# Kernel optimization log

Measured on AMD Instinct MI355X. Metric: run time of the kernel, lower is better.

The kernel has to match this reference:

```python
import jax, jax.numpy as jnp
import numpy as np

K = 7
PAD = 3
SIZE = K * K
MAX_STEP = 2
IMG_SIZE = 384
EPS = 1e-5


def _unfold(x, k, pad):
    # x: (n, c, h, w) -> (n, c, k*k, h*w), same layout as F.unfold with stride 1
    n, c, h, w = x.shape
    xp = jnp.pad(x, ((0, 0), (0, 0), (pad, pad), (pad, pad)))
    patches = jnp.stack(
        [xp[:, :, i:i + h, j:j + w] for i in range(k) for j in range(k)], axis=2
    )  # (n, c, k*k, h, w)
    return patches.reshape(n, c, k * k, h * w)


def setup_inputs() -> dict:
    key = jax.random.key(0)
    k1, k2, k3, k4 = jax.random.split(key, 4)
    n, c, h, w = 1, 256, 96, 96
    inputs = {
        "input": jax.random.normal(k1, (n, c, h, w), dtype=jnp.float32),
        "weight": jax.random.uniform(k2, (n, SIZE, h * w), dtype=jnp.float32),
        "conv_w": jax.random.normal(k3, (3, c), dtype=jnp.float32) * 0.05,
        "conv_b": jax.random.normal(k4, (3,), dtype=jnp.float32) * 0.05,
    }
    return inputs


def reference(input, weight, conv_w, conv_b):
    n, c, h, w = input.shape
    wc = weight.shape[1] // SIZE  # 1 -> broadcasts over channels
    wgt = weight.reshape(n, wc, SIZE, h * w)
    # row-normalize per-pixel window weights (sym_norm=False branch)
    norm_weight = wgt / (jnp.sum(wgt, axis=2, keepdims=True) + EPS)
    x = input
    for _ in range(MAX_STEP):
        p = _unfold(x, K, PAD)                  # (n, c, k*k, h*w)
        x = (p * norm_weight).sum(axis=2).reshape(n, c, h, w)
    # 1x1 conv latent_dim -> 3
    x = jnp.einsum("nchw,oc->nohw", x, conv_w) + conv_b[None, :, None, None]
    # bilinear upsample, half-pixel centers (== torch align_corners=False)
    x = jax.image.resize(x, (n, 3, IMG_SIZE, IMG_SIZE), method="bilinear")
    return x
```

## Files before the change

kernel.cpp:

```cpp
#include <hip/hip_runtime.h>

#define HW 9216
#define W 96
#define H 96
#define NC 256
#define NT 49
#define EPSV 1e-5f

#define TS 16
#define HSZ 22
#define CC 8
#define NZ (NC / CC)

typedef _Float16 half8 __attribute__((ext_vector_type(8)));

template <int FUSE_CONV>
__global__ __launch_bounds__(256) void step_kernel(const float* __restrict__ x,
                                                   const float* __restrict__ w,
                                                   const float* __restrict__ cw,
                                                   float* __restrict__ y) {
    __shared__ half8 xs[HSZ][HSZ];
    const int tx = threadIdx.x & 15;
    const int ty = threadIdx.x >> 4;
    const int bx = blockIdx.x * TS;
    const int by = blockIdx.y * TS;
    const int px = bx + tx;
    const int py = by + ty;
    const int p = py * W + px;

    float wreg[NT];
    float s = 0.f;
#pragma unroll
    for (int t = 0; t < NT; ++t) { wreg[t] = w[t * HW + p]; s += wreg[t]; }
    const float inv = 1.f / (s + EPSV);
#pragma unroll
    for (int t = 0; t < NT; ++t) wreg[t] *= inv;

    const int cbase = blockIdx.z * CC;
    const float* __restrict__ xb = x + cbase * HW;
    for (int i = threadIdx.x; i < HSZ * HSZ; i += 256) {
        int hy = i / HSZ;
        int hx = i - hy * HSZ;
        int gy = by - 3 + hy;
        int gx = bx - 3 + hx;
        half8 h;
#pragma unroll
        for (int c = 0; c < 8; ++c) h[c] = (_Float16)0.f;
        if ((unsigned)gy < (unsigned)H && (unsigned)gx < (unsigned)W) {
            const float* sp = xb + gy * W + gx;
#pragma unroll
            for (int c = 0; c < 8; ++c) h[c] = (_Float16)sp[c * HW];
        }
        xs[hy][hx] = h;
    }
    __syncthreads();

    float acc[8];
#pragma unroll
    for (int k = 0; k < 8; ++k) acc[k] = 0.f;

#pragma unroll
    for (int i = 0; i < 7; ++i) {
#pragma unroll
        for (int j = 0; j < 7; ++j) {
            const float wv = wreg[i * 7 + j];
            const half8 v = xs[ty + i][tx + j];
#pragma unroll
            for (int k = 0; k < 8; ++k)
                acc[k] = fmaf((float)v[k], wv, acc[k]);
        }
    }

    if (FUSE_CONV) {
        float o0 = 0.f, o1 = 0.f, o2 = 0.f;
#pragma unroll
        for (int k = 0; k < 8; ++k) {
            const int c = cbase + k;
            o0 = fmaf(acc[k], cw[c], o0);
            o1 = fmaf(acc[k], cw[NC + c], o1);
            o2 = fmaf(acc[k], cw[2 * NC + c], o2);
        }
        const int z = blockIdx.z;
        y[(z * 3 + 0) * HW + p] = o0;
        y[(z * 3 + 1) * HW + p] = o1;
        y[(z * 3 + 2) * HW + p] = o2;
    } else {
#pragma unroll
        for (int k = 0; k < 8; ++k)
            y[(cbase + k) * HW + p] = acc[k];
    }
}

#define OUTS 384
#define SRCP 10
__global__ __launch_bounds__(256) void upsample_kernel(const float* __restrict__ partial,
                                                       const float* __restrict__ cb,
                                                       float* __restrict__ dst) {
    __shared__ float cvs[3][SRCP][SRCP];
    const int X = blockIdx.x * 32;
    const int Y = blockIdx.y * 32;
    const int x0s = X >> 2;
    const int y0s = Y >> 2;

    for (int e = threadIdx.x; e < 3 * SRCP * SRCP; e += 256) {
        int ch = e / (SRCP * SRCP);
        int r = e - ch * (SRCP * SRCP);
        int sy = r / SRCP;
        int sx = r - sy * SRCP;
        int gy = min(max(y0s - 1 + sy, 0), H - 1);
        int gx = min(max(x0s - 1 + sx, 0), W - 1);
        const int p = gy * W + gx;
        float sum = cb[ch];
#pragma unroll
        for (int z = 0; z < NZ; ++z) sum += partial[(z * 3 + ch) * HW + p];
        cvs[ch][sy][sx] = sum;
    }
    __syncthreads();

    const int xl = threadIdx.x & 31;
    const int yl0 = threadIdx.x >> 5;
    const int xo = X + xl;
    const float sxf = xo * 0.25f - 0.375f;
    const float fxf = floorf(sxf);
    const int jx = (int)fxf - (x0s - 1);
    const float fx = sxf - fxf;

#pragma unroll
    for (int k = 0; k < 4; ++k) {
        const int yo = Y + yl0 + 8 * k;
        const float syf = yo * 0.25f - 0.375f;
        const float fyf = floorf(syf);
        const int jy = (int)fyf - (y0s - 1);
        const float fy = syf - fyf;
#pragma unroll
        for (int ch = 0; ch < 3; ++ch) {
            const float v00 = cvs[ch][jy][jx], v01 = cvs[ch][jy][jx + 1];
            const float v10 = cvs[ch][jy + 1][jx], v11 = cvs[ch][jy + 1][jx + 1];
            const float v0 = v00 + (v01 - v00) * fx;
            const float v1 = v10 + (v11 - v10) * fx;
            dst[ch * OUTS * OUTS + yo * OUTS + xo] = v0 + (v1 - v0) * fy;
        }
    }
}

extern "C" void kernel_launch(void* const* d_in, const int* in_sizes, int n_in,
                              void* d_out, int out_size, void* d_ws, size_t ws_size,
                              hipStream_t stream) {
    const float* input  = (const float*)d_in[0];
    const float* weight = (const float*)d_in[1];
    const float* conv_w = (const float*)d_in[2];
    const float* conv_b = (const float*)d_in[3];
    float* out = (float*)d_out;

    float* ws = (float*)d_ws;
    float* x1      = ws;
    float* partial = x1 + NC * HW;

    dim3 g(W / TS, H / TS, NZ);
    step_kernel<0><<<g, 256, 0, stream>>>(input, weight, nullptr, x1);
    step_kernel<1><<<g, 256, 0, stream>>>(x1, weight, conv_w, partial);

    dim3 gu(OUTS / 32, OUTS / 32);
    upsample_kernel<<<gu, 256, 0, stream>>>(partial, conv_b, out);
}
```

Measured before the change: 35.59 us.

## Prepack inputs and normalized weights to fp16 in a separate pre-pass kernel

Adds a pack kernel that converts the input to a channel-interleaved fp16 layout (8 channels per pixel) and precomputes the normalized window weights once as fp16 pairs. The step kernels then load halo tiles with one 16-byte vector load per pixel instead of eight strided fp32 loads, and they no longer recompute weight normalization in each of the 64 blocks per pixel. The intermediate after the first step is stored in fp16. The cost is an extra kernel launch and pass over the input, plus reduced weight precision from fp16 rounding.

```diff
diff --git a/kernel.cpp b/kernel.cpp
--- a/kernel.cpp
+++ b/kernel.cpp
@@ -5,20 +5,52 @@
 #define H 96
 #define NC 256
 #define NT 49
+#define NPAIR 25
 #define EPSV 1e-5f
 
 #define TS 16
 #define HSZ 22
 #define CC 8
-#define NZ (NC / CC)
+#define NZ 32
 
 typedef _Float16 half8 __attribute__((ext_vector_type(8)));
+typedef _Float16 half2v __attribute__((ext_vector_type(2)));
+
+__global__ __launch_bounds__(256) void pack_kernel(const float* __restrict__ x,
+                                                   const float* __restrict__ w,
+                                                   _Float16* __restrict__ xpack,
+                                                   half2v* __restrict__ nwh) {
+    if (blockIdx.y < 8) {
+        const int g = blockIdx.y * 4 + (threadIdx.x >> 6);
+        const int px = blockIdx.x * 64 + (threadIdx.x & 63);
+        const float* __restrict__ sp = x + (size_t)(g * 8) * HW + px;
+        half8 h;
+#pragma unroll
+        for (int c = 0; c < 8; ++c) h[c] = (_Float16)sp[c * HW];
+        *(half8*)(xpack + ((size_t)g * HW + px) * 8) = h;
+    } else {
+        if (blockIdx.x >= 36) return;
+        const int p = blockIdx.x * 256 + threadIdx.x;
+        float wv[NT];
+        float s = 0.f;
+#pragma unroll
+        for (int t = 0; t < NT; ++t) { wv[t] = w[t * HW + p]; s += wv[t]; }
+        const float inv = 1.f / (s + EPSV);
+#pragma unroll
+        for (int i = 0; i < NPAIR; ++i) {
+            half2v h;
+            h[0] = (_Float16)(wv[2 * i] * inv);
+            h[1] = (2 * i + 1 < NT) ? (_Float16)(wv[2 * i + 1] * inv) : (_Float16)0.f;
+            nwh[i * HW + p] = h;
+        }
+    }
+}
 
 template <int FUSE_CONV>
-__global__ __launch_bounds__(256) void step_kernel(const float* __restrict__ x,
-                                                   const float* __restrict__ w,
+__global__ __launch_bounds__(256) void step_kernel(const _Float16* __restrict__ xin,
+                                                   const half2v* __restrict__ nwh,
                                                    const float* __restrict__ cw,
-                                                   float* __restrict__ y) {
+                                                   void* __restrict__ yout) {
     __shared__ half8 xs[HSZ][HSZ];
     const int tx = threadIdx.x & 15;
     const int ty = threadIdx.x >> 4;
@@ -27,31 +59,28 @@
     const int px = bx + tx;
     const int py = by + ty;
     const int p = py * W + px;
-
-    float wreg[NT];
-    float s = 0.f;
-#pragma unroll
-    for (int t = 0; t < NT; ++t) { wreg[t] = w[t * HW + p]; s += wreg[t]; }
-    const float inv = 1.f / (s + EPSV);
-#pragma unroll
-    for (int t = 0; t < NT; ++t) wreg[t] *= inv;
-
-    const int cbase = blockIdx.z * CC;
-    const float* __restrict__ xb = x + cbase * HW;
-    for (int i = threadIdx.x; i < HSZ * HSZ; i += 256) {
-        int hy = i / HSZ;
-        int hx = i - hy * HSZ;
-        int gy = by - 3 + hy;
-        int gx = bx - 3 + hx;
-        half8 h;
-#pragma unroll
-        for (int c = 0; c < 8; ++c) h[c] = (_Float16)0.f;
-        if ((unsigned)gy < (unsigned)H && (unsigned)gx < (unsigned)W) {
-            const float* sp = xb + gy * W + gx;
-#pragma unroll
-            for (int c = 0; c < 8; ++c) h[c] = (_Float16)sp[c * HW];
-        }
-        xs[hy][hx] = h;
+    const int z = blockIdx.z;
+
+    half2v wu[NPAIR];
+#pragma unroll
+    for (int i = 0; i < NPAIR; ++i) wu[i] = nwh[i * HW + p];
+
+    const _Float16* __restrict__ xz = xin + (size_t)z * HW * 8;
+#pragma unroll
+    for (int it = 0; it < 2; ++it) {
+        const int i = threadIdx.x + it * 256;
+        if (i < HSZ * HSZ) {
+            const int hy = i / HSZ;
+            const int hx = i - hy * HSZ;
+            const int gy = by - 3 + hy;
+            const int gx = bx - 3 + hx;
+            half8 v;
+#pragma unroll
+            for (int c = 0; c < 8; ++c) v[c] = (_Float16)0.f;
+            if ((unsigned)gy < (unsigned)H && (unsigned)gx < (unsigned)W)
+                v = *(const half8*)(xz + (size_t)(gy * W + gx) * 8);
+            xs[hy][hx] = v;
+        }
     }
     __syncthreads();
 
@@ -63,16 +92,18 @@
     for (int i = 0; i < 7; ++i) {
 #pragma unroll
         for (int j = 0; j < 7; ++j) {
-            const float wv = wreg[i * 7 + j];
+            const int t = i * 7 + j;
+            const float wf = (float)wu[t >> 1][t & 1];
             const half8 v = xs[ty + i][tx + j];
 #pragma unroll
             for (int k = 0; k < 8; ++k)
-                acc[k] = fmaf((float)v[k], wv, acc[k]);
+                acc[k] = fmaf(wf, (float)v[k], acc[k]);
         }
     }
 
     if (FUSE_CONV) {
         float o0 = 0.f, o1 = 0.f, o2 = 0.f;
+        const int cbase = z * CC;
 #pragma unroll
         for (int k = 0; k < 8; ++k) {
             const int c = cbase + k;
@@ -80,14 +111,16 @@
             o1 = fmaf(acc[k], cw[NC + c], o1);
             o2 = fmaf(acc[k], cw[2 * NC + c], o2);
         }
-        const int z = blockIdx.z;
-        y[(z * 3 + 0) * HW + p] = o0;
-        y[(z * 3 + 1) * HW + p] = o1;
-        y[(z * 3 + 2) * HW + p] = o2;
+        float* __restrict__ part = (float*)yout;
+        part[(z * 3 + 0) * HW + p] = o0;
+        part[(z * 3 + 1) * HW + p] = o1;
+        part[(z * 3 + 2) * HW + p] = o2;
     } else {
-#pragma unroll
-        for (int k = 0; k < 8; ++k)
-            y[(cbase + k) * HW + p] = acc[k];
+        half8 h;
+#pragma unroll
+        for (int k = 0; k < 8; ++k) h[k] = (_Float16)acc[k];
+        _Float16* __restrict__ yo = (_Float16*)yout;
+        *(half8*)(yo + ((size_t)z * HW + p) * 8) = h;
     }
 }
 
@@ -152,13 +185,18 @@
     const float* conv_b = (const float*)d_in[3];
     float* out = (float*)d_out;
 
-    float* ws = (float*)d_ws;
-    float* x1      = ws;
-    float* partial = x1 + NC * HW;
+    char* ws = (char*)d_ws;
+    _Float16* xpack = (_Float16*)ws;
+    _Float16* x1h   = xpack + (size_t)NZ * HW * 8;
+    half2v*   nwh   = (half2v*)(x1h + (size_t)NZ * HW * 8);
+    float*  partial = (float*)((char*)nwh + (size_t)NPAIR * HW * 4);
+
+    dim3 gp(144, 9);
+    pack_kernel<<<gp, 256, 0, stream>>>(input, weight, xpack, nwh);
 
     dim3 g(W / TS, H / TS, NZ);
-    step_kernel<0><<<g, 256, 0, stream>>>(input, weight, nullptr, x1);
-    step_kernel<1><<<g, 256, 0, stream>>>(x1, weight, conv_w, partial);
+    step_kernel<0><<<g, 256, 0, stream>>>(xpack, nwh, nullptr, (void*)x1h);
+    step_kernel<1><<<g, 256, 0, stream>>>(x1h, nwh, conv_w, (void*)partial);
 
     dim3 gu(OUTS / 32, OUTS / 32);
     upsample_kernel<<<gu, 256, 0, stream>>>(partial, conv_b, out);
```

Result: no change. 36.01 us (+1.2%).
